# Optimization experiments

Measured on AMD Instinct MI355X. Metric: run time of the kernel, lower is better.

The kernel has to match this reference:

```python
import jax, jax.numpy as jnp
import numpy as np

N = 50000      # nodes per type
E = 200000     # edges per relation
H, D = 4, 64   # heads, per-head dim
C = H * D      # hidden = hc_graph * heads = 256
L = 3          # num_hops (HGTConv layers)
HC_LIN, HC_TASK = 256, 128
OUT_DIMS = (3, 3, 3, 5, 1, 1, 8)  # ptr_l1/l2/l3, leaf_category, signed, floating, size


def setup_inputs() -> dict:
    key = jax.random.key(0)
    ks = jax.random.split(key, 24)
    f = lambda k, s: jax.random.normal(k, s, dtype=jnp.float32) * 0.05
    ri = lambda k: jax.random.randint(k, (E,), 0, N, dtype=jnp.int32)
    return {
        "xe": f(ks[0], (N, C)),
        "xs": f(ks[1], (N, C)),
        "ee_src": ri(ks[2]), "ee_dst": ri(ks[3]),
        "es_src": ri(ks[4]), "es_dst": ri(ks[5]),
        "se_src": ri(ks[6]), "se_dst": ri(ks[7]),
        # per-layer, per-node-type projections (2 node types)
        "Wk": f(ks[8], (L, 2, C, C)),
        "Wq": f(ks[9], (L, 2, C, C)),
        "Wv": f(ks[10], (L, 2, C, C)),
        "Wa": f(ks[11], (L, 2, C, C)),
        "skip": jnp.ones((L, 2), dtype=jnp.float32),
        # per-layer, per-relation attention/message transforms (3 relations)
        "Arel": f(ks[12], (L, 3, H, D, D)),
        "Mrel": f(ks[13], (L, 3, H, D, D)),
        "mu": jnp.ones((L, 3, H), dtype=jnp.float32),
        # shared linear stack + 7 task heads (final out padded to 8, sliced per head)
        "Wsh": f(ks[14], (2, HC_LIN, HC_LIN)),
        "bsh": jnp.zeros((2, HC_LIN), dtype=jnp.float32),
        "Wt1": f(ks[15], (7, HC_LIN, HC_TASK)),
        "bt1": jnp.zeros((7, HC_TASK), dtype=jnp.float32),
        "Wt2": f(ks[16], (7, HC_TASK, 8)),
        "bt2": jnp.zeros((7, 8), dtype=jnp.float32),
    }


def _seg_softmax(scores, seg, n):
    m = jax.ops.segment_max(scores, seg, num_segments=n)
    e = jnp.exp(scores - m[seg])
    s = jax.ops.segment_sum(e, seg, num_segments=n)
    return e / (s[seg] + 1e-16)


def _hgt_forward(xe, xs, ee_src, ee_dst, es_src, es_dst, se_src, se_dst,
                 Wk, Wq, Wv, Wa, skip, Arel, Mrel, mu, Wsh, bsh, Wt1, bt1, Wt2, bt2):
    inv_sqrt_d = 1.0 / jnp.sqrt(jnp.float32(D))

    def rel(k_src, v_src, q_dst, src, dst, A, M, m):
        kt = jnp.einsum('ehd,hdf->ehf', k_src[src], A)          # [E,H,D]
        score = (q_dst[dst] * kt).sum(-1) * (m * inv_sqrt_d)    # [E,H]
        msg = jnp.einsum('ehd,hdf->ehf', v_src[src], M)         # [E,H,D]
        return score, msg

    for l in range(L):
        ke = (xe @ Wk[l, 0]).reshape(N, H, D)
        qe = (xe @ Wq[l, 0]).reshape(N, H, D)
        ve = (xe @ Wv[l, 0]).reshape(N, H, D)
        ks_ = (xs @ Wk[l, 1]).reshape(N, H, D)
        qs = (xs @ Wq[l, 1]).reshape(N, H, D)
        vs = (xs @ Wv[l, 1]).reshape(N, H, D)

        s0, m0 = rel(ke, ve, qe, ee_src, ee_dst, Arel[l, 0], Mrel[l, 0], mu[l, 0])  # expr->expr
        s1, m1 = rel(ke, ve, qs, es_src, es_dst, Arel[l, 1], Mrel[l, 1], mu[l, 1])  # expr->stmt
        s2, m2 = rel(ks_, vs, qe, se_src, se_dst, Arel[l, 2], Mrel[l, 2], mu[l, 2])  # stmt->expr

        # destination 'expr': softmax over all incoming edges (rel0 + rel2)
        sc_e = jnp.concatenate([s0, s2], axis=0)
        ms_e = jnp.concatenate([m0, m2], axis=0)
        dst_e = jnp.concatenate([ee_dst, se_dst], axis=0)
        a_e = _seg_softmax(sc_e, dst_e, N)
        agg_e = jax.ops.segment_sum(a_e[..., None] * ms_e, dst_e, num_segments=N).reshape(N, C)

        # destination 'stmt': only rel1
        a_s = _seg_softmax(s1, es_dst, N)
        agg_s = jax.ops.segment_sum(a_s[..., None] * m1, es_dst, num_segments=N).reshape(N, C)

        be = jax.nn.sigmoid(skip[l, 0])
        bs = jax.nn.sigmoid(skip[l, 1])
        xe = be * (jax.nn.gelu(agg_e, approximate=False) @ Wa[l, 0]) + (1.0 - be) * xe
        xs = bs * (jax.nn.gelu(agg_s, approximate=False) @ Wa[l, 1]) + (1.0 - bs) * xs

    # shared linear stack on 'expr' nodes
    h = xe
    for i in range(Wsh.shape[0]):
        h = jax.nn.relu(h @ Wsh[i] + bsh[i])

    # 7 task heads: hidden layer + final (padded to 8 outputs, sliced per head)
    t = jax.nn.relu(jnp.einsum('nc,kct->knt', h, Wt1) + bt1[:, None, :])  # [7,N,HC_TASK]
    o = jnp.einsum('knt,kto->kno', t, Wt2) + bt2[:, None, :]              # [7,N,8]
    outs = [o[i, :, :d] for i, d in enumerate(OUT_DIMS)]
    return jnp.concatenate(outs, axis=-1)  # [N, 24]


def reference(xe, xs, ee_src, ee_dst, es_src, es_dst, se_src, se_dst,
              Wk, Wq, Wv, Wa, skip, Arel, Mrel, mu, Wsh, bsh, Wt1, bt1, Wt2, bt2):
    return _hgt_forward(xe, xs, ee_src, ee_dst, es_src, es_dst, se_src, se_dst,
                        Wk, Wq, Wv, Wa, skip, Arel, Mrel, mu, Wsh, bsh, Wt1, bt1, Wt2, bt2)
```

## Files before the change

### kernel.cpp

```cpp
#include <hip/hip_runtime.h>
#include <hip/hip_fp16.h>
#include <cmath>


#define CDIM 256
#define AR_R (256 * 256)

using f16x8 = __attribute__((ext_vector_type(8))) _Float16;
using f16x4 = __attribute__((ext_vector_type(4))) _Float16;
using f16x2 = __attribute__((ext_vector_type(2))) _Float16;
using f32x4 = __attribute__((ext_vector_type(4))) float;

__device__ __forceinline__ float gelu_f(float x) {
    return 0.5f * x * (1.0f + erff(x * 0.70710678118654752f));
}

__device__ __forceinline__ float dot8f(const f16x8 a, const f16x8 b, float r) {
#if __has_builtin(__builtin_amdgcn_fdot2)
#pragma unroll
    for (int t = 0; t < 4; ++t) {
        f16x2 av = {a[2 * t], a[2 * t + 1]};
        f16x2 bv = {b[2 * t], b[2 * t + 1]};
        r = __builtin_amdgcn_fdot2(av, bv, r, false);
    }
#else
#pragma unroll
    for (int t = 0; t < 8; ++t) r += (float)a[t] * (float)b[t];
#endif
    return r;
}

__global__ __launch_bounds__(256) void zero_k(int* __restrict__ p, size_t n) {
    size_t i = (size_t)blockIdx.x * blockDim.x + threadIdx.x;
    const size_t stride = (size_t)gridDim.x * blockDim.x;
    for (; i < n; i += stride) p[i] = 0;
}

__global__ __launch_bounds__(256) void cvt2_k(const float* __restrict__ xe_in,
                                              const float* __restrict__ xs_in,
                                              _Float16* __restrict__ xeH,
                                              _Float16* __restrict__ xsH,
                                              size_t n4) {
    const float* in = blockIdx.y ? xs_in : xe_in;
    _Float16* out = blockIdx.y ? xsH : xeH;
    size_t i = (size_t)blockIdx.x * blockDim.x + threadIdx.x;
    const size_t stride = (size_t)gridDim.x * blockDim.x;
    for (; i < n4; i += stride) {
        const float4 v = ((const float4*)in)[i];
        f16x4 o;
        o[0] = (_Float16)v.x; o[1] = (_Float16)v.y;
        o[2] = (_Float16)v.z; o[3] = (_Float16)v.w;
        ((f16x4*)out)[i] = o;
    }
}

__device__ __forceinline__ void cvtT_dev(const float* __restrict__ W,
                                         _Float16* __restrict__ dst) {
    const int o = blockIdx.x, c = threadIdx.x;
    dst[(size_t)o * 256 + c] = (_Float16)W[(size_t)c * 256 + o];
}

__device__ __forceinline__ void foldT_dev(const float* __restrict__ Wbase,
                                          const float* __restrict__ T,
                                          _Float16* __restrict__ dst) {
    __shared__ float row[256];
    const int c = blockIdx.x, t = threadIdx.x;
    row[t] = Wbase[(size_t)c * 256 + t];
    __syncthreads();
    const int h = t >> 6, f = t & 63;
    const float* Th = T + h * 4096;
    float acc = 0.f;
#pragma unroll 8
    for (int d = 0; d < 64; ++d) acc += row[h * 64 + d] * Th[d * 64 + f];
    dst[(size_t)t * 256 + c] = (_Float16)acc;
}

__global__ __launch_bounds__(256) void prep_layer_k(
    const float* __restrict__ Wk, const float* __restrict__ Wq,
    const float* __restrict__ Wv, const float* __restrict__ Wa,
    const float* __restrict__ Arel, const float* __restrict__ Mrel,
    _Float16* __restrict__ arena) {
    const size_t CC = 65536, HDD = 16384;
    const int l = blockIdx.y / 10;
    const int c = blockIdx.y % 10;
    _Float16* L = arena + (size_t)l * 10 * AR_R;
    const float* Wk0 = Wk + (l * 2 + 0) * CC;
    const float* Wk1 = Wk + (l * 2 + 1) * CC;
    const float* Wv0 = Wv + (l * 2 + 0) * CC;
    const float* Wv1 = Wv + (l * 2 + 1) * CC;
    switch (c) {
        case 0: cvtT_dev(Wq + (l * 2 + 0) * CC, L); break;
        case 1: foldT_dev(Wk0, Arel + (l * 3 + 0) * HDD, L + 1 * AR_R); break;
        case 2: foldT_dev(Wk0, Arel + (l * 3 + 1) * HDD, L + 2 * AR_R); break;
        case 3: cvtT_dev(Wq + (l * 2 + 1) * CC, L + 3 * AR_R); break;
        case 4: foldT_dev(Wk1, Arel + (l * 3 + 2) * HDD, L + 4 * AR_R); break;
        case 5: foldT_dev(Wv0, Mrel + (l * 3 + 0) * HDD, L + 5 * AR_R); break;
        case 6: foldT_dev(Wv0, Mrel + (l * 3 + 1) * HDD, L + 6 * AR_R); break;
        case 7: foldT_dev(Wv1, Mrel + (l * 3 + 2) * HDD, L + 7 * AR_R); break;
        case 8: cvtT_dev(Wa + (l * 2 + 0) * CC, L + 8 * AR_R); break;
        case 9: cvtT_dev(Wa + (l * 2 + 1) * CC, L + 9 * AR_R); break;
    }
}

__global__ __launch_bounds__(256) void prep_stack_k(const float* __restrict__ Wsh,
                                                    _Float16* __restrict__ SA) {
    cvtT_dev(Wsh + (size_t)blockIdx.y * 65536, SA + (size_t)blockIdx.y * AR_R);
}

__global__ __launch_bounds__(256) void prep_heads_k(const float* __restrict__ Wt1,
                                                    _Float16* __restrict__ HA) {
    const int o = blockIdx.x, k = blockIdx.y, c = threadIdx.x;
    HA[(size_t)(k * 128 + o) * 256 + c] =
        (_Float16)Wt1[(size_t)k * 256 * 128 + (size_t)c * 128 + o];
}

template <int EPI, bool SPLIT>
__device__ __forceinline__ void gemm_body(
    const _Float16* __restrict__ A, const _Float16* __restrict__ Bt,
    _Float16* __restrict__ C, int M, int Nc, int bm, int bn, size_t bufStride,
    const float* __restrict__ bias, const float* __restrict__ skipv,
    _Float16* As, _Float16* Bs) {
    const int tid = threadIdx.x;
    const int wave = tid >> 6, lane = tid & 63;
    const int wm = (wave >> 1) * 64, wn = (wave & 1) * 64;
    const int l15 = lane & 15, g = lane >> 4;

    f32x4 acc[4][4] = {};

    for (int k0 = 0; k0 < 256; k0 += 64) {
        __syncthreads();
#pragma unroll
        for (int p = 0; p < 4; ++p) {
            const int slot = p * 256 + tid;
            const int r = slot >> 3;
            const int cb = ((slot & 7) << 4) ^ ((r & 7) << 4);
            int gr = bm + r; if (gr >= M) gr = M - 1;
            __builtin_amdgcn_global_load_lds(
                (const __attribute__((address_space(1))) void*)
                    ((const char*)A + ((size_t)gr * 256 + k0) * 2 + cb),
                (__attribute__((address_space(3))) void*)((char*)As + slot * 16),
                16, 0, 0);
            __builtin_amdgcn_global_load_lds(
                (const __attribute__((address_space(1))) void*)
                    ((const char*)Bt + ((size_t)(bn + r) * 256 + k0) * 2 + cb),
                (__attribute__((address_space(3))) void*)((char*)Bs + slot * 16),
                16, 0, 0);
        }
        __syncthreads();
#pragma unroll
        for (int sub = 0; sub < 2; ++sub) {
            f16x8 af[4], bf[4];
#pragma unroll
            for (int i = 0; i < 4; ++i) {
                const int ra = wm + i * 16 + l15;
                const int rb = wn + i * 16 + l15;
                const int ka = (sub * 64 + g * 16) ^ ((ra & 7) << 4);
                const int kb = (sub * 64 + g * 16) ^ ((rb & 7) << 4);
                af[i] = *(const f16x8*)((const char*)As + ra * 128 + ka);
                bf[i] = *(const f16x8*)((const char*)Bs + rb * 128 + kb);
            }
#pragma unroll
            for (int mi = 0; mi < 4; ++mi)
#pragma unroll
                for (int ni = 0; ni < 4; ++ni)
                    acc[mi][ni] = __builtin_amdgcn_mfma_f32_16x16x32_f16(
                        af[mi], bf[ni], acc[mi][ni], 0, 0, 0);
        }
    }

    float be = 0.f, ombe = 0.f;
    if (EPI == 1) {
        const float s = skipv[0];
        be = 1.0f / (1.0f + expf(-s));
        ombe = 1.0f - be;
    }
#pragma unroll
    for (int mi = 0; mi < 4; ++mi) {
#pragma unroll
        for (int r = 0; r < 4; ++r) {
            const int row = bm + wm + mi * 16 + g * 4 + r;
            if (row >= M) continue;
#pragma unroll
            for (int ni = 0; ni < 4; ++ni) {
                const int colg = bn + wn + ni * 16 + l15;
                float v = acc[mi][ni][r];
                size_t idx;
                if (SPLIT)
                    idx = (size_t)(colg >> 8) * bufStride + (size_t)row * 256 +
                          (colg & 255);
                else
                    idx = (size_t)row * Nc + colg;
                if (EPI == 1) v = be * v + ombe * (float)C[idx];
                if (EPI == 2) v = fmaxf(v + bias[colg], 0.f);
                C[idx] = (_Float16)v;
            }
        }
    }
}

template <int EPI, bool SPLIT>
__global__ __launch_bounds__(256) void gemm_h(
    const _Float16* __restrict__ A, const _Float16* __restrict__ Bt,
    _Float16* __restrict__ C, int M, int Nc, size_t bufStride,
    const float* __restrict__ bias, const float* __restrict__ skipv) {
    __shared__ _Float16 As[128 * 64];
    __shared__ _Float16 Bs[128 * 64];
    gemm_body<EPI, SPLIT>(A, Bt, C, M, Nc, blockIdx.y * 128, blockIdx.x * 128,
                          bufStride, bias, skipv, As, Bs);
}

__global__ __launch_bounds__(256) void projq_k(
    const _Float16* __restrict__ xeH, const _Float16* __restrict__ xsH,
    const _Float16* __restrict__ L, _Float16* __restrict__ Hb, int M) {
    __shared__ _Float16 As[128 * 64];
    __shared__ _Float16 Bs[128 * 64];
    const int job = blockIdx.x >> 1;
    const int bn = (blockIdx.x & 1) * 128;
    const _Float16* A = (job < 3) ? xeH : xsH;
    const _Float16* Bt = L + (size_t)job * AR_R;
    _Float16* C = Hb + (size_t)job * (size_t)M * 256;
    gemm_body<0, false>(A, Bt, C, M, 256, blockIdx.y * 128, bn, 0, nullptr,
                        nullptr, As, Bs);
}

__global__ __launch_bounds__(256) void projv_k(
    const _Float16* __restrict__ xeH, const _Float16* __restrict__ xsH,
    const _Float16* __restrict__ L, _Float16* __restrict__ Hb, int M) {
    __shared__ _Float16 As[128 * 64];
    __shared__ _Float16 Bs[128 * 64];
    const int job = blockIdx.x >> 1;
    const int bn = (blockIdx.x & 1) * 128;
    const _Float16* A = (job < 2) ? xeH : xsH;
    const _Float16* Bt = L + (size_t)(5 + job) * AR_R;
    const int dsti = (job == 0) ? 1 : (job == 1) ? 2 : 4;
    _Float16* C = Hb + (size_t)dsti * (size_t)M * 256;
    gemm_body<0, false>(A, Bt, C, M, 256, blockIdx.y * 128, bn, 0, nullptr,
                        nullptr, As, Bs);
}

__global__ __launch_bounds__(256) void update2_k(
    const _Float16* __restrict__ aggE, const _Float16* __restrict__ aggS,
    const _Float16* __restrict__ WaT0, const _Float16* __restrict__ WaT1,
    _Float16* __restrict__ xeH, _Float16* __restrict__ xsH,
    const float* __restrict__ skipb, int M) {
    __shared__ _Float16 As[128 * 64];
    __shared__ _Float16 Bs[128 * 64];
    const int sel = blockIdx.x >> 1;
    const int bn = (blockIdx.x & 1) * 128;
    const int bm = blockIdx.y * 128;
    if (sel == 0)
        gemm_body<1, false>(aggE, WaT0, xeH, M, 256, bm, bn, 0, nullptr, skipb,
                            As, Bs);
    else
        gemm_body<1, false>(aggS, WaT1, xsH, M, 256, bm, bn, 0, nullptr,
                            skipb + 1, As, Bs);
}

__global__ __launch_bounds__(256) void hist3_k(const int* __restrict__ d0,
                                               const int* __restrict__ d1,
                                               const int* __restrict__ d2,
                                               int* __restrict__ cnt, int N,
                                               int E) {
    const int i = blockIdx.x * 256 + threadIdx.x;
    if (i >= E) return;
    const int r = blockIdx.y;
    const int* d = r == 0 ? d0 : r == 1 ? d1 : d2;
    atomicAdd(&cnt[(size_t)r * N + d[i]], 1);
}

__global__ __launch_bounds__(256) void partial_k(const int* __restrict__ cnt,
                                                 int* __restrict__ partials,
                                                 int N, int PB) {
    const int r = blockIdx.y, b = blockIdx.x, tid = threadIdx.x;
    const int gi = b * 256 + tid;
    int v = (gi < N) ? cnt[(size_t)r * N + gi] : 0;
#pragma unroll
    for (int o = 1; o < 64; o <<= 1) v += __shfl_xor(v, o);
    __shared__ int ws[4];
    if ((tid & 63) == 0) ws[tid >> 6] = v;
    __syncthreads();
    if (tid == 0) partials[r * PB + b] = ws[0] + ws[1] + ws[2] + ws[3];
}

__global__ __launch_bounds__(256) void scanp_k(int* __restrict__ partials,
                                               int* __restrict__ rp, int N,
                                               int PB, int E) {
    __shared__ int lds[256];
    const int r = blockIdx.y, tid = threadIdx.x;
    const int v = (tid < PB) ? partials[r * PB + tid] : 0;
    lds[tid] = v;
    __syncthreads();
    int acc = v;
    for (int off = 1; off < 256; off <<= 1) {
        const int t = (tid >= off) ? lds[tid - off] : 0;
        __syncthreads();
        acc += t;
        lds[tid] = acc;
        __syncthreads();
    }
    if (tid < PB) partials[r * PB + tid] = acc - v;
    if (tid == 0) rp[(size_t)r * (N + 1) + N] = E;
}

__global__ __launch_bounds__(256) void rpwrite_k(const int* __restrict__ cnt,
                                                 const int* __restrict__ partials,
                                                 int* __restrict__ rp, int N,
                                                 int PB) {
    __shared__ int lds[256];
    const int r = blockIdx.y, b = blockIdx.x, tid = threadIdx.x;
    const int gi = b * 256 + tid;
    const int v = (gi < N) ? cnt[(size_t)r * N + gi] : 0;
    lds[tid] = v;
    __syncthreads();
    int acc = v;
    for (int off = 1; off < 256; off <<= 1) {
        const int t = (tid >= off) ? lds[tid - off] : 0;
        __syncthreads();
        acc += t;
        lds[tid] = acc;
        __syncthreads();
    }
    if (gi < N) rp[(size_t)r * (N + 1) + gi] = partials[r * PB + b] + acc - v;
}

__global__ __launch_bounds__(256) void scatter3_k(
    const int* __restrict__ d0, const int* __restrict__ d1,
    const int* __restrict__ d2, const int* __restrict__ s0_,
    const int* __restrict__ s1_, const int* __restrict__ s2_,
    const int* __restrict__ rp, int* __restrict__ fill,
    int* __restrict__ colsrc, int N, int E) {
    const int i = blockIdx.x * 256 + threadIdx.x;
    if (i >= E) return;
    const int r = blockIdx.y;
    const int* d = r == 0 ? d0 : r == 1 ? d1 : d2;
    const int* s = r == 0 ? s0_ : r == 1 ? s1_ : s2_;
    const int dd = d[i];
    const int p = rp[(size_t)r * (N + 1) + dd] + atomicAdd(&fill[(size_t)r * N + dd], 1);
    colsrc[(size_t)r * E + p] = s[i];
}

__device__ __forceinline__ void score_rel_g(
    const f16x8 q0, const f16x8 q1, const _Float16* __restrict__ kA,
    const int* __restrict__ cs, int beg, int end, float scl,
    float* __restrict__ sc, int grp, int j, float& m) {
    for (int i = beg + grp; i < end; i += 4) {
        const int s = cs[i];
        const _Float16* row = &kA[(size_t)s * 256 + j * 16];
        const f16x8 k0 = *(const f16x8*)row;
        const f16x8 k1 = *(const f16x8*)(row + 8);
        float p = dot8f(q1, k1, dot8f(q0, k0, 0.f));
        p += __shfl_xor(p, 1);
        p += __shfl_xor(p, 2);
        const float v = p * scl;
        if ((j & 3) == 0) {
            sc[(size_t)i * 4 + (j >> 2)] = v;
            m = fmaxf(m, v);
        }
    }
}

__global__ __launch_bounds__(256) void score3_k(
    const _Float16* __restrict__ qe, const _Float16* __restrict__ kA0,
    const _Float16* __restrict__ kA1, const _Float16* __restrict__ qs,
    const _Float16* __restrict__ kA2, const int* __restrict__ rp,
    const int* __restrict__ colsrc, const float* __restrict__ muL,
    float* __restrict__ sc, float* __restrict__ mx_e,
    float* __restrict__ mx_s, int N, int E) {
    const int wid = (blockIdx.x * blockDim.x + threadIdx.x) >> 6;
    if (wid >= N) return;
    const int lane = threadIdx.x & 63;
    const int grp = lane >> 4, j = lane & 15, h = j >> 2;
    const size_t E4 = (size_t)E * 4;
    float m = -1e30f;
    if (blockIdx.y == 0) {
        const _Float16* qrow = &qe[(size_t)wid * 256 + j * 16];
        const f16x8 q0 = *(const f16x8*)qrow;
        const f16x8 q1 = *(const f16x8*)(qrow + 8);
        score_rel_g(q0, q1, kA0, colsrc, rp[wid], rp[wid + 1],
                    muL[0 * 4 + h] * 0.125f, sc, grp, j, m);
        const int* rp2 = rp + 2 * (N + 1);
        score_rel_g(q0, q1, kA2, colsrc + 2 * (size_t)E, rp2[wid], rp2[wid + 1],
                    muL[2 * 4 + h] * 0.125f, sc + 2 * E4, grp, j, m);
        m = fmaxf(m, __shfl_xor(m, 16));
        m = fmaxf(m, __shfl_xor(m, 32));
        if (grp == 0 && (j & 3) == 0) mx_e[(size_t)wid * 4 + h] = m;
    } else {
        const _Float16* qrow = &qs[(size_t)wid * 256 + j * 16];
        const f16x8 q0 = *(const f16x8*)qrow;
        const f16x8 q1 = *(const f16x8*)(qrow + 8);
        const int* rp1 = rp + (N + 1);
        score_rel_g(q0, q1, kA1, colsrc + (size_t)E, rp1[wid], rp1[wid + 1],
                    muL[1 * 4 + h] * 0.125f, sc + E4, grp, j, m);
        m = fmaxf(m, __shfl_xor(m, 16));
        m = fmaxf(m, __shfl_xor(m, 32));
        if (grp == 0 && (j & 3) == 0) mx_s[(size_t)wid * 4 + h] = m;
    }
}

__device__ __forceinline__ void agg_rel_on(
    const float* __restrict__ sc, const _Float16* __restrict__ vM,
    const int* __restrict__ cs, int beg, int end, float mh, int grp, int j,
    int h, float* accf, float& den) {
    for (int i = beg + grp; i < end; i += 4) {
        const int s = cs[i];
        const float w = __expf(sc[(size_t)i * 4 + h] - mh);
        den += w;
        const _Float16* row = &vM[(size_t)s * 256 + j * 16];
        const f16x8 v0 = *(const f16x8*)row;
        const f16x8 v1 = *(const f16x8*)(row + 8);
#pragma unroll
        for (int t = 0; t < 8; ++t) accf[t] += w * (float)v0[t];
#pragma unroll
        for (int t = 0; t < 8; ++t) accf[8 + t] += w * (float)v1[t];
    }
}

__global__ __launch_bounds__(256) void agg3_k(
    const float* __restrict__ sc, const _Float16* __restrict__ vM0,
    const _Float16* __restrict__ vM1, const _Float16* __restrict__ vM2,
    const int* __restrict__ rp, const int* __restrict__ colsrc,
    const float* __restrict__ mx_e, const float* __restrict__ mx_s,
    _Float16* __restrict__ outE, _Float16* __restrict__ outS, int N, int E) {
    const int wid = (blockIdx.x * blockDim.x + threadIdx.x) >> 6;
    if (wid >= N) return;
    const int lane = threadIdx.x & 63;
    const int grp = lane >> 4, j = lane & 15, h = j >> 2;
    const size_t E4 = (size_t)E * 4;
    float accf[16] = {};
    float den = 0.f;
    _Float16* outp;
    if (blockIdx.y == 0) {
        const float mh = mx_e[(size_t)wid * 4 + h];
        const int b0 = rp[wid], e0 = rp[wid + 1];
        const int* rp2 = rp + 2 * (N + 1);
        const int b2 = rp2[wid], e2 = rp2[wid + 1];
        agg_rel_on(sc, vM0, colsrc, b0, e0, mh, grp, j, h, accf, den);
        agg_rel_on(sc + 2 * E4, vM2, colsrc + 2 * (size_t)E, b2, e2, mh, grp,
                   j, h, accf, den);
        outp = outE;
    } else {
        const float mh = mx_s[(size_t)wid * 4 + h];
        const int* rp1 = rp + (N + 1);
        const int b1 = rp1[wid], e1 = rp1[wid + 1];
        agg_rel_on(sc + E4, vM1, colsrc + (size_t)E, b1, e1, mh, grp, j, h,
                   accf, den);
        outp = outS;
    }
    den += __shfl_xor(den, 16);
    den += __shfl_xor(den, 32);
#pragma unroll
    for (int t = 0; t < 16; ++t) {
        accf[t] += __shfl_xor(accf[t], 16);
        accf[t] += __shfl_xor(accf[t], 32);
    }
    const float dinv = 1.0f / (den + 1e-16f);
    f16x4 o;
#pragma unroll
    for (int t = 0; t < 4; ++t)
        o[t] = (_Float16)gelu_f(accf[grp * 4 + t] * dinv);
    *(f16x4*)&outp[(size_t)wid * 256 + j * 16 + grp * 4] = o;
}

__global__ __launch_bounds__(256) void head2_k(const _Float16* __restrict__ t,
                                               const float* __restrict__ Wt2,
                                               const float* __restrict__ bt2,
                                               float* __restrict__ out, int M) {
    const int k = blockIdx.y;
    __shared__ float Ws[128 * 8];
    __shared__ float bs[8];
    const int tid = threadIdx.x;
    const float* W2 = Wt2 + (size_t)k * 1024;
    for (int i = tid; i < 1024; i += 256) Ws[i] = W2[i];
    if (tid < 8) bs[tid] = bt2[k * 8 + tid];
    __syncthreads();
    const int OFFA[7] = {0, 3, 6, 9, 14, 15, 16};
    const int DIMSA[7] = {3, 3, 3, 5, 1, 1, 8};
    const int nl = tid >> 3, o = tid & 7;
    const int n = blockIdx.x * 32 + nl;
    if (n >= M) return;
    const _Float16* tr = &t[(size_t)n * 896 + k * 128];
    float acc = bs[o];
#pragma unroll 8
    for (int d = 0; d < 128; ++d) acc += (float)tr[d] * Ws[d * 8 + o];
    if (o < DIMSA[k]) out[(size_t)n * 24 + OFFA[k] + o] = acc;
}


extern "C" void kernel_launch(void* const* d_in, const int* in_sizes, int n_in,
                              void* d_out, int out_size, void* d_ws,
                              size_t ws_size, hipStream_t stream) {
    const float* xe_in = (const float*)d_in[0];
    const float* xs_in = (const float*)d_in[1];
    const int* ee_src = (const int*)d_in[2];
    const int* ee_dst = (const int*)d_in[3];
    const int* es_src = (const int*)d_in[4];
    const int* es_dst = (const int*)d_in[5];
    const int* se_src = (const int*)d_in[6];
    const int* se_dst = (const int*)d_in[7];
    const float* Wk = (const float*)d_in[8];
    const float* Wq = (const float*)d_in[9];
    const float* Wv = (const float*)d_in[10];
    const float* Wa = (const float*)d_in[11];
    const float* skip = (const float*)d_in[12];
    const float* Arel = (const float*)d_in[13];
    const float* Mrel = (const float*)d_in[14];
    const float* mu = (const float*)d_in[15];
    const float* Wsh = (const float*)d_in[16];
    const float* bsh = (const float*)d_in[17];
    const float* Wt1 = (const float*)d_in[18];
    const float* bt1 = (const float*)d_in[19];
    const float* Wt2 = (const float*)d_in[20];
    const float* bt2 = (const float*)d_in[21];
    float* out = (float*)d_out;

    const int N = in_sizes[0] / CDIM;
    const int E = in_sizes[2];
    const size_t NC = (size_t)N * CDIM;
    const size_t E4 = (size_t)E * 4;
    const size_t N4 = (size_t)N * 4;
    const int PB = (N + 255) / 256;

    const size_t halfs = 7 * NC + 32 * (size_t)AR_R + 7 * 32768;
    const size_t floats = 3 * E4 + 2 * N4;
    const size_t ints =
        3 * (size_t)(N + 1) + 3 * (size_t)E + 3 * (size_t)N + 3 * (size_t)PB;
    const size_t need = halfs * 2 + floats * 4 + ints * 4;
    if (ws_size < need) return;

    _Float16* xeH = (_Float16*)d_ws;
    _Float16* xsH = xeH + NC;
    _Float16* Hb = xsH + NC;
    _Float16* H1 = Hb;
    _Float16* H2 = Hb + NC;
    _Float16* H3 = Hb + 2 * NC;
    _Float16* H4 = Hb + 3 * NC;
    _Float16* H5 = Hb + 4 * NC;
    _Float16* arena = Hb + 5 * NC;
    _Float16* SA = arena + (size_t)30 * AR_R;
    _Float16* HA = SA + (size_t)2 * AR_R;
    float* sc = (float*)(HA + (size_t)7 * 32768);
    float* mx_e = sc + 3 * E4;
    float* mx_s = mx_e + N4;
    int* rp = (int*)(mx_s + N4);
    int* colsrc = rp + 3 * (size_t)(N + 1);
    int* cnt = colsrc + 3 * (size_t)E;
    int* partials = cnt + 3 * (size_t)N;

    const int gx = (N + 127) / 128;
    const dim3 e3((E + 255) / 256, 3);
    const dim3 p3(PB, 3);
    const int wave_blocks = (N + 3) / 4;
    const int zc_blocks = (3 * N + 255) / 256;

    zero_k<<<zc_blocks, 256, 0, stream>>>(cnt, 3 * (size_t)N);
    hist3_k<<<e3, 256, 0, stream>>>(ee_dst, es_dst, se_dst, cnt, N, E);
    partial_k<<<p3, 256, 0, stream>>>(cnt, partials, N, PB);
    scanp_k<<<dim3(1, 3), 256, 0, stream>>>(partials, rp, N, PB, E);
    rpwrite_k<<<p3, 256, 0, stream>>>(cnt, partials, rp, N, PB);
    zero_k<<<zc_blocks, 256, 0, stream>>>(cnt, 3 * (size_t)N);
    scatter3_k<<<e3, 256, 0, stream>>>(ee_dst, es_dst, se_dst, ee_src, es_src,
                                       se_src, rp, cnt, colsrc, N, E);

    prep_layer_k<<<dim3(256, 30), 256, 0, stream>>>(Wk, Wq, Wv, Wa, Arel, Mrel,
                                                    arena);
    prep_stack_k<<<dim3(256, 2), 256, 0, stream>>>(Wsh, SA);
    prep_heads_k<<<dim3(128, 7), 256, 0, stream>>>(Wt1, HA);

    cvt2_k<<<dim3(1024, 2), 256, 0, stream>>>(xe_in, xs_in, xeH, xsH, NC / 4);

    for (int l = 0; l < 3; ++l) {
        _Float16* L = arena + (size_t)l * 10 * AR_R;
        projq_k<<<dim3(10, gx), 256, 0, stream>>>(xeH, xsH, L, Hb, N);
        score3_k<<<dim3(wave_blocks, 2), 256, 0, stream>>>(
            H1, H2, H3, H4, H5, rp, colsrc, mu + l * 12, sc, mx_e, mx_s, N, E);
        projv_k<<<dim3(6, gx), 256, 0, stream>>>(xeH, xsH, L, Hb, N);
        agg3_k<<<dim3(wave_blocks, 2), 256, 0, stream>>>(
            sc, H2, H3, H5, rp, colsrc, mx_e, mx_s, H1, H4, N, E);
        update2_k<<<dim3(4, gx), 256, 0, stream>>>(
            H1, H4, L + 8 * AR_R, L + 9 * AR_R, xeH, xsH, skip + l * 2, N);
    }

    gemm_h<2, false><<<dim3(2, gx), 256, 0, stream>>>(xeH, SA, H5, N, 256, 0,
                                                      bsh, nullptr);
    gemm_h<2, false><<<dim3(2, gx), 256, 0, stream>>>(H5, SA + AR_R, xsH, N,
                                                      256, 0, bsh + 256, nullptr);
    gemm_h<2, false><<<dim3(7, gx), 256, 0, stream>>>(xsH, HA, Hb, N, 896, 0,
                                                      bt1, nullptr);
    head2_k<<<dim3((N + 31) / 32, 7), 256, 0, stream>>>(Hb, Wt2, bt2, out, N);
}
```

Baseline: 1.048 ms.

## Split edge score and aggregation kernels across head pairs with two-edge unrolling

The score and aggregation kernels now launch four y-blocks instead of two, so each wavefront handles only half the feature row (two heads, 128 features) for one node. Each lane then loads 8 halves per edge instead of 16, and the edge loops are unrolled by two so two independent gathers are in flight at once. This doubles the wave count to raise memory-level parallelism and cut per-lane register use on these gather-bound kernels. In exchange, the CSR indices and row pointers are read twice and each wave carries more fixed overhead per node.

```diff
diff --git a/kernel.cpp b/kernel.cpp
--- a/kernel.cpp
+++ b/kernel.cpp
@@ -339,23 +339,34 @@
     colsrc[(size_t)r * E + p] = s[i];
 }
 
-__device__ __forceinline__ void score_rel_g(
-    const f16x8 q0, const f16x8 q1, const _Float16* __restrict__ kA,
+__device__ __forceinline__ void score_rel_h(
+    const f16x8 qv, const _Float16* __restrict__ kA,
     const int* __restrict__ cs, int beg, int end, float scl,
-    float* __restrict__ sc, int grp, int j, float& m) {
-    for (int i = beg + grp; i < end; i += 4) {
-        const int s = cs[i];
-        const _Float16* row = &kA[(size_t)s * 256 + j * 16];
-        const f16x8 k0 = *(const f16x8*)row;
-        const f16x8 k1 = *(const f16x8*)(row + 8);
-        float p = dot8f(q1, k1, dot8f(q0, k0, 0.f));
-        p += __shfl_xor(p, 1);
-        p += __shfl_xor(p, 2);
-        const float v = p * scl;
-        if ((j & 3) == 0) {
-            sc[(size_t)i * 4 + (j >> 2)] = v;
-            m = fmaxf(m, v);
+    float* __restrict__ sc, int fo, int j, int grp, int h, float& m) {
+    int i = beg + grp;
+    for (; i + 4 < end; i += 8) {
+        const int s0 = cs[i], s1 = cs[i + 4];
+        const f16x8 k0 = *(const f16x8*)&kA[(size_t)s0 * 256 + fo];
+        const f16x8 k1 = *(const f16x8*)&kA[(size_t)s1 * 256 + fo];
+        float p0 = dot8f(qv, k0, 0.f), p1 = dot8f(qv, k1, 0.f);
+        p0 += __shfl_xor(p0, 1); p1 += __shfl_xor(p1, 1);
+        p0 += __shfl_xor(p0, 2); p1 += __shfl_xor(p1, 2);
+        p0 += __shfl_xor(p0, 4); p1 += __shfl_xor(p1, 4);
+        const float v0 = p0 * scl, v1 = p1 * scl;
+        if ((j & 7) == 0) {
+            sc[(size_t)i * 4 + h] = v0;
+            sc[(size_t)(i + 4) * 4 + h] = v1;
         }
+        m = fmaxf(m, fmaxf(v0, v1));
+    }
+    if (i < end) {
+        const int s0 = cs[i];
+        const f16x8 k0 = *(const f16x8*)&kA[(size_t)s0 * 256 + fo];
+        float p0 = dot8f(qv, k0, 0.f);
+        p0 += __shfl_xor(p0, 1); p0 += __shfl_xor(p0, 2); p0 += __shfl_xor(p0, 4);
+        const float v0 = p0 * scl;
+        if ((j & 7) == 0) sc[(size_t)i * 4 + h] = v0;
+        m = fmaxf(m, v0);
     }
 }
 
@@ -369,49 +380,56 @@
     const int wid = (blockIdx.x * blockDim.x + threadIdx.x) >> 6;
     if (wid >= N) return;
     const int lane = threadIdx.x & 63;
-    const int grp = lane >> 4, j = lane & 15, h = j >> 2;
+    const int grp = lane >> 4, j = lane & 15;
+    const int dom = blockIdx.y >> 1, hp = blockIdx.y & 1;
+    const int h = hp * 2 + (j >> 3);
+    const int fo = hp * 128 + j * 8;
     const size_t E4 = (size_t)E * 4;
     float m = -1e30f;
-    if (blockIdx.y == 0) {
-        const _Float16* qrow = &qe[(size_t)wid * 256 + j * 16];
-        const f16x8 q0 = *(const f16x8*)qrow;
-        const f16x8 q1 = *(const f16x8*)(qrow + 8);
-        score_rel_g(q0, q1, kA0, colsrc, rp[wid], rp[wid + 1],
-                    muL[0 * 4 + h] * 0.125f, sc, grp, j, m);
+    if (dom == 0) {
+        const f16x8 qv = *(const f16x8*)&qe[(size_t)wid * 256 + fo];
+        score_rel_h(qv, kA0, colsrc, rp[wid], rp[wid + 1],
+                    muL[0 * 4 + h] * 0.125f, sc, fo, j, grp, h, m);
         const int* rp2 = rp + 2 * (N + 1);
-        score_rel_g(q0, q1, kA2, colsrc + 2 * (size_t)E, rp2[wid], rp2[wid + 1],
-                    muL[2 * 4 + h] * 0.125f, sc + 2 * E4, grp, j, m);
+        score_rel_h(qv, kA2, colsrc + 2 * (size_t)E, rp2[wid], rp2[wid + 1],
+                    muL[2 * 4 + h] * 0.125f, sc + 2 * E4, fo, j, grp, h, m);
         m = fmaxf(m, __shfl_xor(m, 16));
         m = fmaxf(m, __shfl_xor(m, 32));
-        if (grp == 0 && (j & 3) == 0) mx_e[(size_t)wid * 4 + h] = m;
+        if (grp == 0 && (j & 7) == 0) mx_e[(size_t)wid * 4 + h] = m;
     } else {
-        const _Float16* qrow = &qs[(size_t)wid * 256 + j * 16];
-        const f16x8 q0 = *(const f16x8*)qrow;
-        const f16x8 q1 = *(const f16x8*)(qrow + 8);
+        const f16x8 qv = *(const f16x8*)&qs[(size_t)wid * 256 + fo];
         const int* rp1 = rp + (N + 1);
-        score_rel_g(q0, q1, kA1, colsrc + (size_t)E, rp1[wid], rp1[wid + 1],
-                    muL[1 * 4 + h] * 0.125f, sc + E4, grp, j, m);
+        score_rel_h(qv, kA1, colsrc + (size_t)E, rp1[wid], rp1[wid + 1],
+                    muL[1 * 4 + h] * 0.125f, sc + E4, fo, j, grp, h, m);
         m = fmaxf(m, __shfl_xor(m, 16));
         m = fmaxf(m, __shfl_xor(m, 32));
-        if (grp == 0 && (j & 3) == 0) mx_s[(size_t)wid * 4 + h] = m;
-    }
-}
-
-__device__ __forceinline__ void agg_rel_on(
+        if (grp == 0 && (j & 7) == 0) mx_s[(size_t)wid * 4 + h] = m;
+    }
+}
+
+__device__ __forceinline__ void agg_rel_h(
     const float* __restrict__ sc, const _Float16* __restrict__ vM,
-    const int* __restrict__ cs, int beg, int end, float mh, int grp, int j,
-    int h, float* accf, float& den) {
-    for (int i = beg + grp; i < end; i += 4) {
-        const int s = cs[i];
-        const float w = __expf(sc[(size_t)i * 4 + h] - mh);
-        den += w;
-        const _Float16* row = &vM[(size_t)s * 256 + j * 16];
-        const f16x8 v0 = *(const f16x8*)row;
-        const f16x8 v1 = *(const f16x8*)(row + 8);
-#pragma unroll
-        for (int t = 0; t < 8; ++t) accf[t] += w * (float)v0[t];
-#pragma unroll
-        for (int t = 0; t < 8; ++t) accf[8 + t] += w * (float)v1[t];
+    const int* __restrict__ cs, int beg, int end, float mh, int fo, int h,
+    int grp, float* accf, float& den) {
+    int i = beg + grp;
+    for (; i + 4 < end; i += 8) {
+        const int s0 = cs[i], s1 = cs[i + 4];
+        const float w0 = __expf(sc[(size_t)i * 4 + h] - mh);
+        const float w1 = __expf(sc[(size_t)(i + 4) * 4 + h] - mh);
+        const f16x8 v0 = *(const f16x8*)&vM[(size_t)s0 * 256 + fo];
+        const f16x8 v1 = *(const f16x8*)&vM[(size_t)s1 * 256 + fo];
+        den += w0 + w1;
+#pragma unroll
+        for (int t = 0; t < 8; ++t)
+            accf[t] += w0 * (float)v0[t] + w1 * (float)v1[t];
+    }
+    if (i < end) {
+        const int s0 = cs[i];
+        const float w0 = __expf(sc[(size_t)i * 4 + h] - mh);
+        const f16x8 v0 = *(const f16x8*)&vM[(size_t)s0 * 256 + fo];
+        den += w0;
+#pragma unroll
+        for (int t = 0; t < 8; ++t) accf[t] += w0 * (float)v0[t];
     }
 }
 
@@ -424,41 +442,41 @@
     const int wid = (blockIdx.x * blockDim.x + threadIdx.x) >> 6;
     if (wid >= N) return;
     const int lane = threadIdx.x & 63;
-    const int grp = lane >> 4, j = lane & 15, h = j >> 2;
+    const int grp = lane >> 4, j = lane & 15;
+    const int dom = blockIdx.y >> 1, hp = blockIdx.y & 1;
+    const int h = hp * 2 + (j >> 3);
+    const int fo = hp * 128 + j * 8;
     const size_t E4 = (size_t)E * 4;
-    float accf[16] = {};
+    float accf[8] = {};
     float den = 0.f;
     _Float16* outp;
-    if (blockIdx.y == 0) {
+    if (dom == 0) {
         const float mh = mx_e[(size_t)wid * 4 + h];
         const int b0 = rp[wid], e0 = rp[wid + 1];
         const int* rp2 = rp + 2 * (N + 1);
-        const int b2 = rp2[wid], e2 = rp2[wid + 1];
-        agg_rel_on(sc, vM0, colsrc, b0, e0, mh, grp, j, h, accf, den);
-        agg_rel_on(sc + 2 * E4, vM2, colsrc + 2 * (size_t)E, b2, e2, mh, grp,
-                   j, h, accf, den);
+        agg_rel_h(sc, vM0, colsrc, b0, e0, mh, fo, h, grp, accf, den);
+        agg_rel_h(sc + 2 * E4, vM2, colsrc + 2 * (size_t)E, rp2[wid],
+                  rp2[wid + 1], mh, fo, h, grp, accf, den);
         outp = outE;
     } else {
         const float mh = mx_s[(size_t)wid * 4 + h];
         const int* rp1 = rp + (N + 1);
-        const int b1 = rp1[wid], e1 = rp1[wid + 1];
-        agg_rel_on(sc + E4, vM1, colsrc + (size_t)E, b1, e1, mh, grp, j, h,
-                   accf, den);
+        agg_rel_h(sc + E4, vM1, colsrc + (size_t)E, rp1[wid], rp1[wid + 1], mh,
+                  fo, h, grp, accf, den);
         outp = outS;
     }
     den += __shfl_xor(den, 16);
     den += __shfl_xor(den, 32);
 #pragma unroll
-    for (int t = 0; t < 16; ++t) {
+    for (int t = 0; t < 8; ++t) {
         accf[t] += __shfl_xor(accf[t], 16);
         accf[t] += __shfl_xor(accf[t], 32);
     }
     const float dinv = 1.0f / (den + 1e-16f);
-    f16x4 o;
-#pragma unroll
-    for (int t = 0; t < 4; ++t)
-        o[t] = (_Float16)gelu_f(accf[grp * 4 + t] * dinv);
-    *(f16x4*)&outp[(size_t)wid * 256 + j * 16 + grp * 4] = o;
+    f16x2 o;
+    o[0] = (_Float16)gelu_f(accf[grp * 2 + 0] * dinv);
+    o[1] = (_Float16)gelu_f(accf[grp * 2 + 1] * dinv);
+    *(f16x2*)&outp[(size_t)wid * 256 + fo + grp * 2] = o;
 }
 
 __global__ __launch_bounds__(256) void head2_k(const _Float16* __restrict__ t,
@@ -571,10 +589,10 @@
     for (int l = 0; l < 3; ++l) {
         _Float16* L = arena + (size_t)l * 10 * AR_R;
         projq_k<<<dim3(10, gx), 256, 0, stream>>>(xeH, xsH, L, Hb, N);
-        score3_k<<<dim3(wave_blocks, 2), 256, 0, stream>>>(
+        score3_k<<<dim3(wave_blocks, 4), 256, 0, stream>>>(
             H1, H2, H3, H4, H5, rp, colsrc, mu + l * 12, sc, mx_e, mx_s, N, E);
         projv_k<<<dim3(6, gx), 256, 0, stream>>>(xeH, xsH, L, Hb, N);
-        agg3_k<<<dim3(wave_blocks, 2), 256, 0, stream>>>(
+        agg3_k<<<dim3(wave_blocks, 4), 256, 0, stream>>>(
             sc, H2, H3, H5, rp, colsrc, mx_e, mx_s, H1, H4, N, E);
         update2_k<<<dim3(4, gx), 256, 0, stream>>>(
             H1, H4, L + 8 * AR_R, L + 9 * AR_R, xeH, xsH, skip + l * 2, N);
```

After: 1.202 ms. +14.7%, slower.
